# Performance work log

Hardware: AMD Instinct MI355X
Metric: run time of the kernel (lower is better)

Reference implementation:

```python
import jax, jax.numpy as jnp
import numpy as np

N, K, D = 8192, 256, 64

def setup_inputs() -> dict:
    key = jax.random.key(0)
    k1, k2, k3, k4, k5 = jax.random.split(key, 5)
    x = jax.random.normal(k1, (N, D), dtype=jnp.float32)
    means = 0.001 * jax.random.uniform(k2, (K, D), dtype=jnp.float32)
    diag = jax.random.normal(k3, (1, K, D), dtype=jnp.float32)
    tri = 0.01 * jax.random.normal(k4, (1, K, D, D), dtype=jnp.float32)
    weigh = jax.random.normal(k5, (1, K), dtype=jnp.float32)
    return {"x": x, "means": means, "diag": diag, "tri": tri, "weigh": weigh}

def reference(x, means, diag, tri, weigh):
    d = x.shape[1]
    logC = -d / 2 * jnp.log(jnp.asarray(2 * np.pi, dtype=x.dtype))
    w = jax.nn.log_softmax(weigh, axis=1)                 # [1,K]
    y = x[:, None, :] - means[None, :, :]                 # [N,K,d]
    lv = jnp.tanh(diag)                                   # [1,K,d]
    y = y * lv                                            # [N,K,d]
    L = jnp.tril(tri[0], k=-1)                            # [K,d,d] strictly lower
    y = y + jnp.einsum('kij,nkj->nki', L, y)              # [N,K,d]
    q = jnp.sum(y * y, axis=2)                            # [N,K]
    logdet = jnp.sum(jnp.log(jnp.abs(lv)), axis=2)        # [1,K]
    val = -q / 2 + logdet + w                             # [N,K]
    logpdf = logC + jax.nn.logsumexp(val, axis=-1)        # [N]
    return jnp.mean(-logpdf)                              # scalar
```

## Files before the change

### kernel.cpp

```cpp
#include <hip/hip_runtime.h>
#include <cstdint>
#include <cstddef>

#define NTOT 8192
#define KTOT 256

typedef _Float16 half2v __attribute__((ext_vector_type(2)));
typedef _Float16 half8  __attribute__((ext_vector_type(8)));
typedef float floatx16 __attribute__((ext_vector_type(16)));

static constexpr size_t G_ELEMS   = (size_t)8 * 260 * 64 * 8;
static constexpr size_t OFF_CK    = G_ELEMS * 2;
static constexpr size_t OFF_BPART = OFF_CK + 1024;
static constexpr size_t OFF_VAL   = 2134016;

__device__ __forceinline__ uint16_t f2h(float x) {
  _Float16 h = (_Float16)x;
  return __builtin_bit_cast(uint16_t, h);
}

__device__ __forceinline__ half8 mkh(half2v s, const half2v* rp) {
  union { half2v p[4]; half8 v; } u;
  u.p[0] = s * rp[0]; u.p[1] = s * rp[1]; u.p[2] = s * rp[2]; u.p[3] = s * rp[3];
  return u.v;
}
__device__ __forceinline__ half8 cph(const half2v* rp) {
  union { half2v p[4]; half8 v; } u;
  u.p[0] = rp[0]; u.p[1] = rp[1]; u.p[2] = rp[2]; u.p[3] = rp[3];
  return u.v;
}

__global__ void p1_prep(const float* __restrict__ means, const float* __restrict__ diag,
                        const float* __restrict__ tri, const float* __restrict__ weigh,
                        uint16_t* __restrict__ Gf, float* __restrict__ ck) {
  int k = blockIdx.x;
  int t = threadIdx.x;
  __shared__ float lv[64], ms[64], bv64[64], wred[256];
  __shared__ float Wp[64][68];
  __shared__ float SS[64][65];
  __shared__ float lse_s;

  float wv = weigh[t];
  wred[t] = wv; __syncthreads();
  for (int o = 128; o > 0; o >>= 1) { if (t < o) wred[t] = fmaxf(wred[t], wred[t + o]); __syncthreads(); }
  float wm = wred[0]; __syncthreads();
  wred[t] = __expf(wv - wm); __syncthreads();
  for (int o = 128; o > 0; o >>= 1) { if (t < o) wred[t] += wred[t + o]; __syncthreads(); }
  if (t == 0) lse_s = wm + __logf(wred[0]);

  float logdet0 = 0.f;
  if (t < 64) {
    float d = diag[k * 64 + t];
    float l = tanhf(d);
    lv[t] = l;
    ms[t] = means[k * 64 + t];
    float ld = __logf(fabsf(l));
    #pragma unroll
    for (int o = 32; o > 0; o >>= 1) ld += __shfl_xor(ld, o);
    logdet0 = ld;
  }
  __syncthreads();

  for (int e = 0; e < 16; ++e) {
    int idx = e * 256 + t;
    int i = idx >> 6, c = idx & 63;
    float L = (c < i) ? tri[k * 4096 + idx] : 0.f;
    float w = ((c == i) ? 1.f : 0.f) + L;
    Wp[i][c] = w * lv[c];
  }
  __syncthreads();

  int i0 = (t >> 4) * 4, j0 = (t & 15) * 4;
  float acc[4][4];
  #pragma unroll
  for (int a = 0; a < 4; ++a)
    #pragma unroll
    for (int b = 0; b < 4; ++b) acc[a][b] = 0.f;
  for (int r = 0; r < 64; ++r) {
    float4 av = *(const float4*)&Wp[r][i0];
    float4 bv = *(const float4*)&Wp[r][j0];
    float aa[4] = {av.x, av.y, av.z, av.w};
    float bb[4] = {bv.x, bv.y, bv.z, bv.w};
    #pragma unroll
    for (int a = 0; a < 4; ++a)
      #pragma unroll
      for (int b = 0; b < 4; ++b) acc[a][b] = fmaf(aa[a], bb[b], acc[a][b]);
  }
  #pragma unroll
  for (int a = 0; a < 4; ++a)
    #pragma unroll
    for (int b = 0; b < 4; ++b) SS[i0 + a][j0 + b] = acc[a][b];
  __syncthreads();

  if (t < 64) {
    float b = 0.f;
    for (int j = 0; j < 64; ++j) b = fmaf(SS[t][j], ms[j], b);
    bv64[t] = b;
    float bm = b * ms[t];
    #pragma unroll
    for (int o = 32; o > 0; o >>= 1) bm += __shfl_xor(bm, o);
    if (t == 0) ck[k] = logdet0 + (weigh[k] - lse_s) - 0.5f * bm;
  }
  __syncthreads();

  int k32 = k >> 5, kl = k & 31;
  for (int cc = t; cc < 520; cc += 256) {
    float v[8];
    if (cc < 512) {
      int i = cc >> 3, jb = (cc & 7) * 8;
      #pragma unroll
      for (int e = 0; e < 8; ++e) v[e] = -0.5f * SS[i][jb + e];
    } else {
      int b0 = (cc - 512) * 8;
      #pragma unroll
      for (int e = 0; e < 8; ++e) v[e] = bv64[b0 + e];
    }
    uint4 pk;
    pk.x = (uint32_t)f2h(v[0]) | ((uint32_t)f2h(v[1]) << 16);
    pk.y = (uint32_t)f2h(v[2]) | ((uint32_t)f2h(v[3]) << 16);
    pk.z = (uint32_t)f2h(v[4]) | ((uint32_t)f2h(v[5]) << 16);
    pk.w = (uint32_t)f2h(v[6]) | ((uint32_t)f2h(v[7]) << 16);
    size_t base = ((size_t)(k32 * 260 + (cc >> 1)) * 64 + (cc & 1) * 32 + kl) * 8;
    *(uint4*)(Gf + base) = pk;
  }
}

__launch_bounds__(256)
__global__ void k2_gemm(const float* __restrict__ x, const uint16_t* __restrict__ Gf,
                        const float* __restrict__ ck, float* __restrict__ val2) {
  __shared__ float xl[128][65];
  int t = threadIdx.x;
  int bx = blockIdx.x, by = blockIdx.y;
  const float* xblk = x + (size_t)bx * (128 * 64);

  for (int e = 0; e < 8; ++e) {
    int lin = e * 1024 + t * 4;
    float4 v = *(const float4*)(xblk + lin);
    int r = lin >> 6, c = lin & 63;
    xl[r][c] = v.x; xl[r][c + 1] = v.y; xl[r][c + 2] = v.z; xl[r][c + 3] = v.w;
  }
  __syncthreads();

  int wave = t >> 6, l = t & 63;
  int wn = wave >> 1, wk = wave & 1;
  int half = l >> 5, lane31 = l & 31;
  int r0 = wn * 64 + lane31, r1 = r0 + 32;

  half2v runh0[4][4], runh1[4][4];
  #pragma unroll
  for (int c = 0; c < 4; ++c) {
    int base = c * 16 + half * 8;
    float4 ra = *(const float4*)(xblk + (size_t)r0 * 64 + base);
    float4 rb = *(const float4*)(xblk + (size_t)r0 * 64 + base + 4);
    runh0[c][0][0] = (_Float16)ra.x; runh0[c][0][1] = (_Float16)ra.y;
    runh0[c][1][0] = (_Float16)ra.z; runh0[c][1][1] = (_Float16)ra.w;
    runh0[c][2][0] = (_Float16)rb.x; runh0[c][2][1] = (_Float16)rb.y;
    runh0[c][3][0] = (_Float16)rb.z; runh0[c][3][1] = (_Float16)rb.w;
    float4 rc = *(const float4*)(xblk + (size_t)r1 * 64 + base);
    float4 rd = *(const float4*)(xblk + (size_t)r1 * 64 + base + 4);
    runh1[c][0][0] = (_Float16)rc.x; runh1[c][0][1] = (_Float16)rc.y;
    runh1[c][1][0] = (_Float16)rc.z; runh1[c][1][1] = (_Float16)rc.w;
    runh1[c][2][0] = (_Float16)rd.x; runh1[c][2][1] = (_Float16)rd.y;
    runh1[c][3][0] = (_Float16)rd.z; runh1[c][3][1] = (_Float16)rd.w;
  }

  int k32 = by * 2 + wk;
  const uint4* Bp = (const uint4*)Gf;
  size_t bofs = (size_t)(k32 * 260) * 64 + l;

  floatx16 acc0, acc1;
  #pragma unroll
  for (int i = 0; i < 16; ++i) { acc0[i] = 0.f; acc1[i] = 0.f; }

  uint4 bufs[4][4];
  #pragma unroll
  for (int p = 0; p < 4; ++p)
    #pragma unroll
    for (int c = 0; c < 4; ++c) bufs[p][c] = Bp[bofs + (size_t)(p * 4 + c) * 64];

  for (int g = 0; g < 64; g += 4) {
    #pragma unroll
    for (int p = 0; p < 4; ++p) {
      int gg = g + p;
      float xf0 = xl[r0][gg], xf1 = xl[r1][gg];
      _Float16 h0 = (_Float16)xf0; half2v xi0; xi0[0] = h0; xi0[1] = h0;
      _Float16 h1 = (_Float16)xf1; half2v xi1; xi1[0] = h1; xi1[1] = h1;
      #pragma unroll
      for (int c = 0; c < 4; ++c) {
        half8 a0 = mkh(xi0, runh0[c]);
        half8 a1 = mkh(xi1, runh1[c]);
        half8 bb = __builtin_bit_cast(half8, bufs[p][c]);
        acc0 = __builtin_amdgcn_mfma_f32_32x32x16_f16(a0, bb, acc0, 0, 0, 0);
        acc1 = __builtin_amdgcn_mfma_f32_32x32x16_f16(a1, bb, acc1, 0, 0, 0);
      }
      #pragma unroll
      for (int c = 0; c < 4; ++c)
        bufs[p][c] = Bp[bofs + (size_t)((gg + 4) * 4 + c) * 64];
    }
  }

  #pragma unroll
  for (int c = 0; c < 4; ++c) {
    half8 a0 = cph(runh0[c]);
    half8 a1 = cph(runh1[c]);
    half8 bb = __builtin_bit_cast(half8, bufs[0][c]);
    acc0 = __builtin_amdgcn_mfma_f32_32x32x16_f16(a0, bb, acc0, 0, 0, 0);
    acc1 = __builtin_amdgcn_mfma_f32_32x32x16_f16(a1, bb, acc1, 0, 0, 0);
  }

  __syncthreads();
  float ckv = ck[by * 64 + wk * 32 + lane31];
  #pragma unroll
  for (int reg = 0; reg < 16; ++reg) {
    int row = (reg & 3) + 8 * (reg >> 2) + 4 * half;
    xl[wn * 64 + row][wk * 32 + lane31] = acc0[reg] + ckv;
    xl[wn * 64 + 32 + row][wk * 32 + lane31] = acc1[reg] + ckv;
  }
  __syncthreads();
  if (t < 128) {
    float m = -3.0e38f;
    #pragma unroll
    for (int j = 0; j < 64; ++j) m = fmaxf(m, xl[t][j]);
    float s = 0.f;
    #pragma unroll
    for (int j = 0; j < 64; ++j) s += __expf(xl[t][j] - m);
    size_t n = (size_t)bx * 128 + t;
    val2[n * 8 + by * 2 + 0] = m;
    val2[n * 8 + by * 2 + 1] = s;
  }
}

__global__ void k3_lse(const float* __restrict__ val2, float* __restrict__ bpart) {
  __shared__ float red[4];
  int t = threadIdx.x;
  size_t n = (size_t)blockIdx.x * 256 + t;
  const float4* p = (const float4*)(val2 + n * 8);
  float4 a = p[0], b = p[1];
  float M = fmaxf(fmaxf(a.x, a.z), fmaxf(b.x, b.z));
  float s = a.y * __expf(a.x - M) + a.w * __expf(a.z - M) +
            b.y * __expf(b.x - M) + b.w * __expf(b.z - M);
  float lse = M + __logf(s);
  #pragma unroll
  for (int o = 32; o > 0; o >>= 1) lse += __shfl_xor(lse, o);
  if ((t & 63) == 0) red[t >> 6] = lse;
  __syncthreads();
  if (t == 0) bpart[blockIdx.x] = red[0] + red[1] + red[2] + red[3];
}

__global__ void k4_final(const float* __restrict__ bpart, float* __restrict__ out) {
  int t = threadIdx.x;
  float v = (t < 32) ? bpart[t] : 0.f;
  #pragma unroll
  for (int o = 32; o > 0; o >>= 1) v += __shfl_xor(v, o);
  if (t == 0) out[0] = 58.8120661251f - v / 8192.0f;
}

extern "C" void kernel_launch(void* const* d_in, const int* in_sizes, int n_in,
                              void* d_out, int out_size, void* d_ws, size_t ws_size,
                              hipStream_t stream) {
  const float* x     = (const float*)d_in[0];
  const float* means = (const float*)d_in[1];
  const float* diag  = (const float*)d_in[2];
  const float* tri   = (const float*)d_in[3];
  const float* weigh = (const float*)d_in[4];

  char* ws = (char*)d_ws;
  uint16_t* Gf  = (uint16_t*)ws;
  float* ck     = (float*)(ws + OFF_CK);
  float* bpart  = (float*)(ws + OFF_BPART);
  float* val2   = (float*)(ws + OFF_VAL);

  p1_prep<<<dim3(256), dim3(256), 0, stream>>>(means, diag, tri, weigh, Gf, ck);
  k2_gemm<<<dim3(64, 4), dim3(256), 0, stream>>>(x, Gf, ck, val2);
  k3_lse<<<dim3(32), dim3(256), 0, stream>>>(val2, bpart);
  k4_final<<<dim3(1), dim3(64), 0, stream>>>(bpart, (float*)d_out);
}
```

Baseline: 101.0 us.

## Exploit symmetry of quadratic form to skip half the MFMA tiles; fuse final reduction

```diff
diff --git a/kernel.cpp b/kernel.cpp
--- a/kernel.cpp
+++ b/kernel.cpp
@@ -9,10 +9,11 @@
 typedef _Float16 half8  __attribute__((ext_vector_type(8)));
 typedef float floatx16 __attribute__((ext_vector_type(16)));
 
-static constexpr size_t G_ELEMS   = (size_t)8 * 260 * 64 * 8;
-static constexpr size_t OFF_CK    = G_ELEMS * 2;
-static constexpr size_t OFF_BPART = OFF_CK + 1024;
-static constexpr size_t OFF_VAL   = 2134016;
+static constexpr int    NJOBS   = 164;
+static constexpr size_t G_ELEMS = (size_t)8 * NJOBS * 64 * 8;
+static constexpr size_t OFF_CK  = G_ELEMS * 2;
+static constexpr size_t OFF_CTR = OFF_CK + 1024;
+static constexpr size_t OFF_VAL = OFF_CK + 4096;
 
 __device__ __forceinline__ uint16_t f2h(float x) {
   _Float16 h = (_Float16)x;
@@ -32,13 +33,16 @@
 
 __global__ void p1_prep(const float* __restrict__ means, const float* __restrict__ diag,
                         const float* __restrict__ tri, const float* __restrict__ weigh,
-                        uint16_t* __restrict__ Gf, float* __restrict__ ck) {
+                        uint16_t* __restrict__ Gf, float* __restrict__ ck,
+                        unsigned int* __restrict__ ctr, float* __restrict__ facc) {
   int k = blockIdx.x;
   int t = threadIdx.x;
   __shared__ float lv[64], ms[64], bv64[64], wred[256];
   __shared__ float Wp[64][68];
   __shared__ float SS[64][65];
   __shared__ float lse_s;
+
+  if (k == 0 && t == 0) { *ctr = 0u; *facc = 0.f; }
 
   float wv = weigh[t];
   wred[t] = wv; __syncthreads();
@@ -104,14 +108,25 @@
   __syncthreads();
 
   int k32 = k >> 5, kl = k & 31;
-  for (int cc = t; cc < 520; cc += 256) {
+  for (int hc = t; hc < 328; hc += 256) {
     float v[8];
-    if (cc < 512) {
-      int i = cc >> 3, jb = (cc & 7) * 8;
-      #pragma unroll
-      for (int e = 0; e < 8; ++e) v[e] = -0.5f * SS[i][jb + e];
+    int job, half = hc & 1;
+    if (hc < 320) {
+      job = hc >> 1;
+      int pp = job / 5, q = job - pp * 5;
+      int i, c;
+      if (pp < 16) { if (q < 4) { i = pp; c = q; } else { i = 63 - pp; c = 3; } }
+      else         { if (q < 3) { i = pp; c = q + 1; } else { i = 63 - pp; c = q - 1; } }
+      int jb = c * 16 + half * 8;
+      #pragma unroll
+      for (int e = 0; e < 8; ++e) {
+        int j = jb + e;
+        float s = SS[i][j];
+        v[e] = (j < i) ? 0.f : ((j == i) ? -0.5f * s : -s);
+      }
     } else {
-      int b0 = (cc - 512) * 8;
+      job = 160 + ((hc - 320) >> 1);
+      int b0 = (hc - 320) * 8;
       #pragma unroll
       for (int e = 0; e < 8; ++e) v[e] = bv64[b0 + e];
     }
@@ -120,7 +135,7 @@
     pk.y = (uint32_t)f2h(v[2]) | ((uint32_t)f2h(v[3]) << 16);
     pk.z = (uint32_t)f2h(v[4]) | ((uint32_t)f2h(v[5]) << 16);
     pk.w = (uint32_t)f2h(v[6]) | ((uint32_t)f2h(v[7]) << 16);
-    size_t base = ((size_t)(k32 * 260 + (cc >> 1)) * 64 + (cc & 1) * 32 + kl) * 8;
+    size_t base = ((size_t)(k32 * NJOBS + job) * 64 + half * 32 + kl) * 8;
     *(uint4*)(Gf + base) = pk;
   }
 }
@@ -166,36 +181,80 @@
 
   int k32 = by * 2 + wk;
   const uint4* Bp = (const uint4*)Gf;
-  size_t bofs = (size_t)(k32 * 260) * 64 + l;
+  size_t bofs = (size_t)(k32 * NJOBS) * 64 + l;
 
   floatx16 acc0, acc1;
   #pragma unroll
   for (int i = 0; i < 16; ++i) { acc0[i] = 0.f; acc1[i] = 0.f; }
 
-  uint4 bufs[4][4];
-  #pragma unroll
-  for (int p = 0; p < 4; ++p)
-    #pragma unroll
-    for (int c = 0; c < 4; ++c) bufs[p][c] = Bp[bofs + (size_t)(p * 4 + c) * 64];
-
-  for (int g = 0; g < 64; g += 4) {
-    #pragma unroll
-    for (int p = 0; p < 4; ++p) {
-      int gg = g + p;
-      float xf0 = xl[r0][gg], xf1 = xl[r1][gg];
-      _Float16 h0 = (_Float16)xf0; half2v xi0; xi0[0] = h0; xi0[1] = h0;
-      _Float16 h1 = (_Float16)xf1; half2v xi1; xi1[0] = h1; xi1[1] = h1;
-      #pragma unroll
-      for (int c = 0; c < 4; ++c) {
-        half8 a0 = mkh(xi0, runh0[c]);
-        half8 a1 = mkh(xi1, runh1[c]);
-        half8 bb = __builtin_bit_cast(half8, bufs[p][c]);
-        acc0 = __builtin_amdgcn_mfma_f32_32x32x16_f16(a0, bb, acc0, 0, 0, 0);
-        acc1 = __builtin_amdgcn_mfma_f32_32x32x16_f16(a1, bb, acc1, 0, 0, 0);
-      }
-      #pragma unroll
-      for (int c = 0; c < 4; ++c)
-        bufs[p][c] = Bp[bofs + (size_t)((gg + 4) * 4 + c) * 64];
+  uint4 bufs[4][5];
+  #pragma unroll
+  for (int s = 0; s < 4; ++s)
+    #pragma unroll
+    for (int q = 0; q < 5; ++q) bufs[s][q] = Bp[bofs + (size_t)(s * 5 + q) * 64];
+
+  #pragma unroll
+  for (int pp = 0; pp < 16; ++pp) {
+    const int s = pp & 3;
+    float xa0f = xl[r0][pp],      xa1f = xl[r1][pp];
+    float xb0f = xl[r0][63 - pp], xb1f = xl[r1][63 - pp];
+    _Float16 ha0 = (_Float16)xa0f; half2v ya0; ya0[0] = ha0; ya0[1] = ha0;
+    _Float16 ha1 = (_Float16)xa1f; half2v ya1; ya1[0] = ha1; ya1[1] = ha1;
+    _Float16 hb0 = (_Float16)xb0f; half2v yb0; yb0[0] = hb0; yb0[1] = hb0;
+    _Float16 hb1 = (_Float16)xb1f; half2v yb1; yb1[0] = hb1; yb1[1] = hb1;
+    #pragma unroll
+    for (int c = 0; c < 4; ++c) {
+      half8 a0 = mkh(ya0, runh0[c]);
+      half8 a1 = mkh(ya1, runh1[c]);
+      half8 bb = __builtin_bit_cast(half8, bufs[s][c]);
+      acc0 = __builtin_amdgcn_mfma_f32_32x32x16_f16(a0, bb, acc0, 0, 0, 0);
+      acc1 = __builtin_amdgcn_mfma_f32_32x32x16_f16(a1, bb, acc1, 0, 0, 0);
+    }
+    {
+      half8 a0 = mkh(yb0, runh0[3]);
+      half8 a1 = mkh(yb1, runh1[3]);
+      half8 bb = __builtin_bit_cast(half8, bufs[s][4]);
+      acc0 = __builtin_amdgcn_mfma_f32_32x32x16_f16(a0, bb, acc0, 0, 0, 0);
+      acc1 = __builtin_amdgcn_mfma_f32_32x32x16_f16(a1, bb, acc1, 0, 0, 0);
+    }
+    #pragma unroll
+    for (int q = 0; q < 5; ++q)
+      bufs[s][q] = Bp[bofs + (size_t)((pp + 4) * 5 + q) * 64];
+  }
+
+  #pragma unroll
+  for (int pp = 16; pp < 32; ++pp) {
+    const int s = pp & 3;
+    float xa0f = xl[r0][pp],      xa1f = xl[r1][pp];
+    float xb0f = xl[r0][63 - pp], xb1f = xl[r1][63 - pp];
+    _Float16 ha0 = (_Float16)xa0f; half2v ya0; ya0[0] = ha0; ya0[1] = ha0;
+    _Float16 ha1 = (_Float16)xa1f; half2v ya1; ya1[0] = ha1; ya1[1] = ha1;
+    _Float16 hb0 = (_Float16)xb0f; half2v yb0; yb0[0] = hb0; yb0[1] = hb0;
+    _Float16 hb1 = (_Float16)xb1f; half2v yb1; yb1[0] = hb1; yb1[1] = hb1;
+    #pragma unroll
+    for (int c = 1; c < 4; ++c) {
+      half8 a0 = mkh(ya0, runh0[c]);
+      half8 a1 = mkh(ya1, runh1[c]);
+      half8 bb = __builtin_bit_cast(half8, bufs[s][c - 1]);
+      acc0 = __builtin_amdgcn_mfma_f32_32x32x16_f16(a0, bb, acc0, 0, 0, 0);
+      acc1 = __builtin_amdgcn_mfma_f32_32x32x16_f16(a1, bb, acc1, 0, 0, 0);
+    }
+    #pragma unroll
+    for (int c = 2; c < 4; ++c) {
+      half8 a0 = mkh(yb0, runh0[c]);
+      half8 a1 = mkh(yb1, runh1[c]);
+      half8 bb = __builtin_bit_cast(half8, bufs[s][c + 1]);
+      acc0 = __builtin_amdgcn_mfma_f32_32x32x16_f16(a0, bb, acc0, 0, 0, 0);
+      acc1 = __builtin_amdgcn_mfma_f32_32x32x16_f16(a1, bb, acc1, 0, 0, 0);
+    }
+    if (pp <= 27) {
+      #pragma unroll
+      for (int q = 0; q < 5; ++q)
+        bufs[s][q] = Bp[bofs + (size_t)((pp + 4) * 5 + q) * 64];
+    } else if (pp == 28) {
+      #pragma unroll
+      for (int q = 0; q < 4; ++q)
+        bufs[s][q] = Bp[bofs + (size_t)(160 + q) * 64];
     }
   }
 
@@ -230,7 +289,8 @@
   }
 }
 
-__global__ void k3_lse(const float* __restrict__ val2, float* __restrict__ bpart) {
+__global__ void k3_lse(const float* __restrict__ val2, float* __restrict__ facc,
+                       unsigned int* __restrict__ ctr, float* __restrict__ out) {
   __shared__ float red[4];
   int t = threadIdx.x;
   size_t n = (size_t)blockIdx.x * 256 + t;
@@ -244,15 +304,16 @@
   for (int o = 32; o > 0; o >>= 1) lse += __shfl_xor(lse, o);
   if ((t & 63) == 0) red[t >> 6] = lse;
   __syncthreads();
-  if (t == 0) bpart[blockIdx.x] = red[0] + red[1] + red[2] + red[3];
-}
-
-__global__ void k4_final(const float* __restrict__ bpart, float* __restrict__ out) {
-  int t = threadIdx.x;
-  float v = (t < 32) ? bpart[t] : 0.f;
-  #pragma unroll
-  for (int o = 32; o > 0; o >>= 1) v += __shfl_xor(v, o);
-  if (t == 0) out[0] = 58.8120661251f - v / 8192.0f;
+  if (t == 0) {
+    float part = red[0] + red[1] + red[2] + red[3];
+    atomicAdd(facc, part);
+    __threadfence();
+    unsigned int rank = atomicAdd(ctr, 1u);
+    if (rank == 31) {
+      float total = atomicAdd(facc, 0.0f);
+      out[0] = 58.8120661251f - total / 8192.0f;
+    }
+  }
 }
 
 extern "C" void kernel_launch(void* const* d_in, const int* in_sizes, int n_in,
@@ -265,13 +326,13 @@
   const float* weigh = (const float*)d_in[4];
 
   char* ws = (char*)d_ws;
-  uint16_t* Gf  = (uint16_t*)ws;
-  float* ck     = (float*)(ws + OFF_CK);
-  float* bpart  = (float*)(ws + OFF_BPART);
-  float* val2   = (float*)(ws + OFF_VAL);
-
-  p1_prep<<<dim3(256), dim3(256), 0, stream>>>(means, diag, tri, weigh, Gf, ck);
+  uint16_t* Gf       = (uint16_t*)ws;
+  float* ck          = (float*)(ws + OFF_CK);
+  unsigned int* ctr  = (unsigned int*)(ws + OFF_CTR);
+  float* facc        = (float*)(ws + OFF_CTR + 4);
+  float* val2        = (float*)(ws + OFF_VAL);
+
+  p1_prep<<<dim3(256), dim3(256), 0, stream>>>(means, diag, tri, weigh, Gf, ck, ctr, facc);
   k2_gemm<<<dim3(64, 4), dim3(256), 0, stream>>>(x, Gf, ck, val2);
-  k3_lse<<<dim3(32), dim3(256), 0, stream>>>(val2, bpart);
-  k4_final<<<dim3(1), dim3(64), 0, stream>>>(bpart, (float*)d_out);
-}
+  k3_lse<<<dim3(32), dim3(256), 0, stream>>>(val2, facc, ctr, (float*)d_out);
+}
```

Measured after the change: 93.26 us, median of 3. 1.08x faster.
